# Kernel tuning notes

Hardware: AMD Instinct MI355X
Metric: run time of the kernel (lower is better)

Reference implementation:

```python
import jax, jax.numpy as jnp
import numpy as np

THRESH = 0.5
ALPHA = 1.0
LOG_CLAMP = -100.0  # torch BCELoss clamps log terms at -100


def setup_inputs() -> dict:
    key = jax.random.key(0)
    k1, k2 = jax.random.split(key)
    B, N, C = 2048, 2704, 5
    # predictions: confidences/boxes in (0,1) (post-sigmoid style)
    x = jax.random.uniform(k1, (B, N, C), dtype=jnp.float32, minval=1e-3, maxval=1.0 - 1e-3)
    # labels: conf in [0,1] (~half > 0.5 -> faces), boxes in [0,1]
    y = jax.random.uniform(k2, (B, N, C), dtype=jnp.float32)
    return {"x": x, "y": y}


def _clog(v):
    return jnp.maximum(jnp.log(v), LOG_CLAMP)


def reference(x, y):
    # x, y: [B, N, 5]; channel 0 = confidence, 1:5 = box
    mask = y[..., 0] > THRESH                      # [B, N] face cells
    face_num = jnp.sum(mask).astype(x.dtype)
    bg_num = mask.size - face_num
    scale = 1.0 + 1.0 / face_num

    # MSE over masked boxes, mean over (face_num * 4) elements
    sq = jnp.sum((x[..., 1:5] - y[..., 1:5]) ** 2, axis=-1)   # [B, N]
    diff_box = scale * jnp.sum(jnp.where(mask, sq, 0.0)) / (face_num * 4.0)

    # BCE(pred_conf, label_conf) over face cells, mean
    p = x[..., 0]
    t = y[..., 0]
    bce = -(t * _clog(p) + (1.0 - t) * _clog(1.0 - p))        # [B, N]
    diff_c = scale * jnp.sum(jnp.where(mask, bce, 0.0)) / face_num

    # BCE(pred_conf, 0) over background cells, mean
    bg_bce = -_clog(1.0 - p)                                  # [B, N]
    diff_bg = ALPHA * jnp.sum(jnp.where(mask, 0.0, bg_bce)) / bg_num

    return diff_box + diff_c + diff_bg
```

## Files before the change

### kernel.cpp

```cpp
#include <hip/hip_runtime.h>


#define BLOCK 256
#define IPT 4
#define LOG_CLAMP -100.0f

__device__ __forceinline__ float clogf(float v) {
    return fmaxf(logf(v), LOG_CLAMP);
}

__global__ __launch_bounds__(BLOCK) void mloss_reduce(
    const float* __restrict__ x, const float* __restrict__ y,
    float4* __restrict__ partials, long long n_groups)
{
    const long long base = (long long)blockIdx.x * (BLOCK * IPT) + threadIdx.x;

    float s_sq = 0.0f, s_bce = 0.0f, s_bg = 0.0f, s_cnt = 0.0f;

    #pragma unroll
    for (int k = 0; k < IPT; ++k) {
        const long long g = base + (long long)k * BLOCK;
        if (g >= n_groups) break;
        const long long e0 = g * 4;
        const int r = (int)(e0 % 5);

        const float4 x4 = ((const float4*)x)[g];
        const float4 y4 = ((const float4*)y)[g];
        const float  yc = y[e0 - r];

        const int jc = (5 - r) % 5;
        const float tnext = (jc == 0) ? y4.x : (jc == 1) ? y4.y : (jc == 2) ? y4.z : y4.w;
        const float pconf = (jc == 0) ? x4.x : (jc == 1) ? x4.y : (jc == 2) ? x4.z : x4.w;
        const bool  has_conf = (r != 1);

        const float lp  = clogf(pconf);
        const float l1p = clogf(1.0f - pconf);
        const bool  mc  = tnext > 0.5f;
        s_bce += (has_conf && mc)  ? -(tnext * lp + (1.0f - tnext) * l1p) : 0.0f;
        s_bg  += (has_conf && !mc) ? -l1p : 0.0f;
        s_cnt += (has_conf && mc)  ? 1.0f : 0.0f;

        #define MLOSS_BOX(J, XJ, YJ) do {                                     \
            const int   m  = r + (J);                                         \
            const bool  ic = (m == 0) || (m == 5);                            \
            const float tj = (m >= 5) ? tnext : yc;                           \
            const float d  = (XJ) - (YJ);                                     \
            s_sq += (!ic && tj > 0.5f) ? d * d : 0.0f;                        \
        } while (0)
        MLOSS_BOX(0, x4.x, y4.x);
        MLOSS_BOX(1, x4.y, y4.y);
        MLOSS_BOX(2, x4.z, y4.z);
        MLOSS_BOX(3, x4.w, y4.w);
        #undef MLOSS_BOX
    }

    #pragma unroll
    for (int off = 32; off > 0; off >>= 1) {
        s_sq  += __shfl_down(s_sq,  off, 64);
        s_bce += __shfl_down(s_bce, off, 64);
        s_bg  += __shfl_down(s_bg,  off, 64);
        s_cnt += __shfl_down(s_cnt, off, 64);
    }

    __shared__ float4 r_part[BLOCK / 64];
    const int wave = threadIdx.x >> 6;
    const int lane = threadIdx.x & 63;
    if (lane == 0) r_part[wave] = make_float4(s_sq, s_bce, s_bg, s_cnt);
    __syncthreads();
    if (threadIdx.x == 0) {
        float4 t0 = r_part[0];
        #pragma unroll
        for (int w = 1; w < BLOCK / 64; ++w) {
            t0.x += r_part[w].x; t0.y += r_part[w].y;
            t0.z += r_part[w].z; t0.w += r_part[w].w;
        }
        partials[blockIdx.x] = t0;
    }
}

#define FBLOCK 1024
__global__ __launch_bounds__(FBLOCK) void mloss_final(
    const float4* __restrict__ partials, int n_parts,
    const float* __restrict__ x, const float* __restrict__ y,
    float* __restrict__ out, long long elem_start, long long n_elems,
    long long n_cells)
{
    double s_sq = 0.0, s_bce = 0.0, s_bg = 0.0, s_cnt = 0.0;
    for (int i = threadIdx.x; i < n_parts; i += FBLOCK) {
        const float4 v = partials[i];
        s_sq += (double)v.x; s_bce += (double)v.y;
        s_bg += (double)v.z; s_cnt += (double)v.w;
    }

    #pragma unroll
    for (int off = 32; off > 0; off >>= 1) {
        s_sq  += __shfl_down(s_sq,  off, 64);
        s_bce += __shfl_down(s_bce, off, 64);
        s_bg  += __shfl_down(s_bg,  off, 64);
        s_cnt += __shfl_down(s_cnt, off, 64);
    }

    __shared__ double r[FBLOCK / 64][4];
    const int wave = threadIdx.x >> 6;
    const int lane = threadIdx.x & 63;
    if (lane == 0) { r[wave][0] = s_sq; r[wave][1] = s_bce; r[wave][2] = s_bg; r[wave][3] = s_cnt; }
    __syncthreads();

    if (threadIdx.x == 0) {
        double t_sq = 0.0, t_bce = 0.0, t_bg = 0.0, face = 0.0;
        #pragma unroll
        for (int w = 0; w < FBLOCK / 64; ++w) {
            t_sq += r[w][0]; t_bce += r[w][1]; t_bg += r[w][2]; face += r[w][3];
        }
        for (long long e = elem_start; e < n_elems; ++e) {
            const long long m  = e % 5;
            const long long cb = e - m;
            const float t_cell = y[cb];
            const bool  mask   = t_cell > 0.5f;
            if (m == 0) {
                const float p   = x[e];
                const float lp  = clogf(p);
                const float l1p = clogf(1.0f - p);
                if (mask) { t_bce += (double)(-(t_cell * lp + (1.0f - t_cell) * l1p)); face += 1.0; }
                else      { t_bg  += (double)(-l1p); }
            } else if (mask) {
                const float d = x[e] - y[e];
                t_sq += (double)(d * d);
            }
        }
        const double bg    = (double)n_cells - face;
        const double scale = 1.0 + 1.0 / face;
        *out = (float)(scale * t_sq / (face * 4.0) + scale * t_bce / face + t_bg / bg);
    }
}

extern "C" void kernel_launch(void* const* d_in, const int* in_sizes, int n_in,
                              void* d_out, int out_size, void* d_ws, size_t ws_size,
                              hipStream_t stream) {
    const float* x = (const float*)d_in[0];
    const float* y = (const float*)d_in[1];
    float* out = (float*)d_out;
    float4* partials = (float4*)d_ws;

    const long long n_elems  = (long long)in_sizes[0];
    const long long n_cells  = n_elems / 5;
    const long long n_groups = n_elems / 4;
    const long long covered  = n_groups * 4;

    const long long gpb    = (long long)BLOCK * IPT;
    const int       blocks = (int)((n_groups + gpb - 1) / gpb);

    mloss_reduce<<<blocks, BLOCK, 0, stream>>>(x, y, partials, n_groups);
    mloss_final<<<1, FBLOCK, 0, stream>>>(partials, blocks, x, y, out,
                                          covered, n_elems, n_cells);
}
```

Measured before the change: 237.2 us.

## Use a persistent grid-stride reduction with batched vector loads and a shuffle-based cell-label lookup

The reduction kernel becomes a persistent grid-stride loop over chunks, with the grid capped at 2048 blocks. Each thread issues all of its x and y vector loads up front, and the x loads are nontemporal. The per-thread scalar gather of the cell's confidence label is replaced by a wavefront shuffle from the neighbouring lane, so only lane 0 does an extra scalar load. Indexing moves from 64-bit to 32-bit, which removes the long modulo. The aim is to cut redundant uncoalesced loads and integer overhead; the cost is more complex lane-dependent logic and relying on 32-bit indices fitting the input size.

```diff
diff --git a/kernel.cpp b/kernel.cpp
--- a/kernel.cpp
+++ b/kernel.cpp
@@ -2,8 +2,10 @@
 
 
 #define BLOCK 256
-#define IPT 4
+#define TPC 4
 #define LOG_CLAMP -100.0f
+
+typedef float nvec4 __attribute__((ext_vector_type(4)));
 
 __device__ __forceinline__ float clogf(float v) {
     return fmaxf(logf(v), LOG_CLAMP);
@@ -11,47 +13,68 @@
 
 __global__ __launch_bounds__(BLOCK) void mloss_reduce(
     const float* __restrict__ x, const float* __restrict__ y,
-    float4* __restrict__ partials, long long n_groups)
+    float4* __restrict__ partials, int n_chunks)
 {
-    const long long base = (long long)blockIdx.x * (BLOCK * IPT) + threadIdx.x;
+    const int lane = threadIdx.x & 63;
+    const int wv   = threadIdx.x >> 6;
+
+    const nvec4*  gx4 = (const nvec4*)x;
+    const float4* gy4 = (const float4*)y;
 
     float s_sq = 0.0f, s_bce = 0.0f, s_bg = 0.0f, s_cnt = 0.0f;
 
-    #pragma unroll
-    for (int k = 0; k < IPT; ++k) {
-        const long long g = base + (long long)k * BLOCK;
-        if (g >= n_groups) break;
-        const long long e0 = g * 4;
-        const int r = (int)(e0 % 5);
+    for (int c = blockIdx.x; c < n_chunks; c += gridDim.x) {
+        int    rr[TPC];
+        nvec4  x4[TPC];
+        float4 y4[TPC];
+        float  yc0[TPC];
+        #pragma unroll
+        for (int k = 0; k < TPC; ++k) {
+            const int g  = (c * TPC + k) * 256 + wv * 64 + lane;
+            const int e0 = g * 4;
+            const int r  = e0 % 5;
+            rr[k] = r;
+            x4[k] = __builtin_nontemporal_load(&gx4[g]);
+            y4[k] = gy4[g];
+            yc0[k] = (lane == 0 && r != 0) ? y[e0 - r] : 0.0f;
+        }
 
-        const float4 x4 = ((const float4*)x)[g];
-        const float4 y4 = ((const float4*)y)[g];
-        const float  yc = y[e0 - r];
+        #pragma unroll
+        for (int k = 0; k < TPC; ++k) {
+            const int    r = rr[k];
+            const nvec4  X = x4[k];
+            const float4 Y = y4[k];
 
-        const int jc = (5 - r) % 5;
-        const float tnext = (jc == 0) ? y4.x : (jc == 1) ? y4.y : (jc == 2) ? y4.z : y4.w;
-        const float pconf = (jc == 0) ? x4.x : (jc == 1) ? x4.y : (jc == 2) ? x4.z : x4.w;
-        const bool  has_conf = (r != 1);
+            const int jc = (5 - r) % 5;
+            const float tnext = (jc == 0) ? Y.x : (jc == 1) ? Y.y : (jc == 2) ? Y.z : Y.w;
+            const float pconf = (jc == 0) ? X.x : (jc == 1) ? X.y : (jc == 2) ? X.z : X.w;
+            const bool  has_conf = (r != 1);
 
-        const float lp  = clogf(pconf);
-        const float l1p = clogf(1.0f - pconf);
-        const bool  mc  = tnext > 0.5f;
-        s_bce += (has_conf && mc)  ? -(tnext * lp + (1.0f - tnext) * l1p) : 0.0f;
-        s_bg  += (has_conf && !mc) ? -l1p : 0.0f;
-        s_cnt += (has_conf && mc)  ? 1.0f : 0.0f;
+            const float lp  = clogf(pconf);
+            const float l1p = clogf(1.0f - pconf);
+            const bool  mc  = tnext > 0.5f;
+            s_bce += (has_conf && mc)  ? -(tnext * lp + (1.0f - tnext) * l1p) : 0.0f;
+            s_bg  += (has_conf && !mc) ? -l1p : 0.0f;
+            s_cnt += (has_conf && mc)  ? 1.0f : 0.0f;
 
-        #define MLOSS_BOX(J, XJ, YJ) do {                                     \
-            const int   m  = r + (J);                                         \
-            const bool  ic = (m == 0) || (m == 5);                            \
-            const float tj = (m >= 5) ? tnext : yc;                           \
-            const float d  = (XJ) - (YJ);                                     \
-            s_sq += (!ic && tj > 0.5f) ? d * d : 0.0f;                        \
-        } while (0)
-        MLOSS_BOX(0, x4.x, y4.x);
-        MLOSS_BOX(1, x4.y, y4.y);
-        MLOSS_BOX(2, x4.z, y4.z);
-        MLOSS_BOX(3, x4.w, y4.w);
-        #undef MLOSS_BOX
+            const float outv = (r == 0) ? Y.x : (r == 2) ? Y.w : (r == 3) ? Y.z : Y.y;
+            float ycp = __shfl_up(outv, 1, 64);
+            if (lane == 0) ycp = yc0[k];
+            const float yc = (r == 0) ? Y.x : ycp;
+
+            #define MLOSS_BOX(J, XJ, YJ) do {                                 \
+                const int   m  = r + (J);                                     \
+                const bool  ic = (m == 0) || (m == 5);                        \
+                const float tj = (m >= 5) ? tnext : yc;                       \
+                const float d  = (XJ) - (YJ);                                 \
+                s_sq += (!ic && tj > 0.5f) ? d * d : 0.0f;                    \
+            } while (0)
+            MLOSS_BOX(0, X.x, Y.x);
+            MLOSS_BOX(1, X.y, Y.y);
+            MLOSS_BOX(2, X.z, Y.z);
+            MLOSS_BOX(3, X.w, Y.w);
+            #undef MLOSS_BOX
+        }
     }
 
     #pragma unroll
@@ -61,11 +84,8 @@
         s_bg  += __shfl_down(s_bg,  off, 64);
         s_cnt += __shfl_down(s_cnt, off, 64);
     }
-
     __shared__ float4 r_part[BLOCK / 64];
-    const int wave = threadIdx.x >> 6;
-    const int lane = threadIdx.x & 63;
-    if (lane == 0) r_part[wave] = make_float4(s_sq, s_bce, s_bg, s_cnt);
+    if (lane == 0) r_part[wv] = make_float4(s_sq, s_bce, s_bg, s_cnt);
     __syncthreads();
     if (threadIdx.x == 0) {
         float4 t0 = r_part[0];
@@ -114,8 +134,7 @@
         }
         for (long long e = elem_start; e < n_elems; ++e) {
             const long long m  = e % 5;
-            const long long cb = e - m;
-            const float t_cell = y[cb];
+            const float t_cell = y[e - m];
             const bool  mask   = t_cell > 0.5f;
             if (m == 0) {
                 const float p   = x[e];
@@ -145,12 +164,14 @@
     const long long n_elems  = (long long)in_sizes[0];
     const long long n_cells  = n_elems / 5;
     const long long n_groups = n_elems / 4;
-    const long long covered  = n_groups * 4;
+    const long long n_tiles  = n_groups / 256;
+    const int       n_chunks = (int)(n_tiles / TPC);
+    const long long covered  = (long long)n_chunks * TPC * 256 * 4;
 
-    const long long gpb    = (long long)BLOCK * IPT;
-    const int       blocks = (int)((n_groups + gpb - 1) / gpb);
+    const int NB = (n_chunks < 2048) ? (n_chunks > 0 ? n_chunks : 1) : 2048;
 
-    mloss_reduce<<<blocks, BLOCK, 0, stream>>>(x, y, partials, n_groups);
-    mloss_final<<<1, FBLOCK, 0, stream>>>(partials, blocks, x, y, out,
-                                          covered, n_elems, n_cells);
+    if (n_chunks > 0)
+        mloss_reduce<<<NB, BLOCK, 0, stream>>>(x, y, partials, n_chunks);
+    mloss_final<<<1, FBLOCK, 0, stream>>>(partials, (n_chunks > 0) ? NB : 0,
+                                          x, y, out, covered, n_elems, n_cells);
 }
```

Measured after the change: 227.5 us. 4.1% less time.
